# Optimization experiments

Measured on AMD Instinct MI355X. Metric: run time of the kernel, lower is better.

Reference implementation:

```python
import jax, jax.numpy as jnp
import numpy as np

D = 1024      # d_model
H = 16        # n_heads
M = 64        # n_memories
DK = D // H   # head dim
EPS = 1e-5    # LayerNorm eps


def setup_inputs() -> dict:
    key = jax.random.key(0)
    ks = jax.random.split(key, 16)
    B, N = 4, 1024
    s = 0.02
    return {
        "queries": jax.random.normal(ks[0], (B, N, D), jnp.float32),
        "keys": jax.random.normal(ks[1], (B, N, D), jnp.float32),
        "values": jax.random.normal(ks[2], (B, N, D), jnp.float32),
        "attention_mask": jax.random.randint(ks[3], (B, 1, 1, N), 0, 2, dtype=jnp.int32),
        "Wq": jax.random.normal(ks[4], (D, D), jnp.float32) * s,
        "bq": jnp.zeros((D,), jnp.float32),
        "Wk": jax.random.normal(ks[5], (D, D), jnp.float32) * s,
        "bk": jnp.zeros((D,), jnp.float32),
        "Wv": jax.random.normal(ks[6], (D, D), jnp.float32) * s,
        "bv": jnp.zeros((D,), jnp.float32),
        "Wo": jax.random.normal(ks[7], (D, D), jnp.float32) * s,
        "bo": jnp.zeros((D,), jnp.float32),
        "m_k": jax.random.normal(ks[8], (1, M, D), jnp.float32) * 0.01,
        "m_v": jax.random.normal(ks[9], (1, M, D), jnp.float32) * 0.01,
        "gamma": jnp.ones((D,), jnp.float32),
        "beta": jnp.zeros((D,), jnp.float32),
    }


def _layer_norm(x, gamma, beta):
    mu = jnp.mean(x, axis=-1, keepdims=True)
    var = jnp.var(x, axis=-1, keepdims=True)
    return (x - mu) * jax.lax.rsqrt(var + EPS) * gamma + beta


def reference(queries, keys, values, attention_mask,
              Wq, bq, Wk, bk, Wv, bv, Wo, bo, m_k, m_v, gamma, beta):
    B, Nq, _ = queries.shape
    Nk = keys.shape[1]
    scale = 1.0 / np.sqrt(DK)

    # projections (torch Linear: x @ W.T + b)
    q = (queries @ Wq.T + bq).reshape(B, Nq, H, DK).transpose(0, 2, 1, 3)  # b h nq d

    # memory-augmented K/V (memory tokens scaled as in the source)
    k_full = jnp.concatenate(
        [keys @ Wk.T + bk, jnp.broadcast_to(m_k * np.sqrt(DK), (B, M, D))], axis=1)
    v_full = jnp.concatenate(
        [values @ Wv.T + bv, jnp.broadcast_to(m_v * np.sqrt(M), (B, M, D))], axis=1)
    k = k_full.reshape(B, Nk + M, H, DK).transpose(0, 2, 1, 3)  # b h nk+m d
    v = v_full.reshape(B, Nk + M, H, DK).transpose(0, 2, 1, 3)  # b h nk+m d

    scores = jnp.einsum('bhqd,bhkd->bhqk', q, k) * scale  # [B,H,Nq,Nk+M]

    # partial masking: only the first Nk (non-memory) columns are maskable
    mask = jnp.concatenate(
        [attention_mask.astype(bool),
         jnp.zeros((B, 1, 1, M), dtype=bool)], axis=-1)
    scores = jnp.where(mask, -jnp.inf, scores)

    p_attn = jax.nn.softmax(scores, axis=-1)  # dropout p=0.0 -> identity
    out = jnp.einsum('bhqk,bhkd->bhqd', p_attn, v)
    out = out.transpose(0, 2, 1, 3).reshape(B, Nq, D)
    out = out @ Wo.T + bo

    # residual + LayerNorm (outer dropout is identity at p=0.0)
    return _layer_norm(queries + out, gamma, beta)
```

## Files before the change

kernel.cpp:

```cpp
#include <hip/hip_runtime.h>


typedef __bf16 bf16;
typedef __bf16 bf16x8 __attribute__((ext_vector_type(8)));
typedef __bf16 bf16x4 __attribute__((ext_vector_type(4)));
typedef __bf16 bf16x2 __attribute__((ext_vector_type(2)));
typedef float  f32x4  __attribute__((ext_vector_type(4)));
typedef float  f32x16 __attribute__((ext_vector_type(16)));
typedef unsigned uintx4 __attribute__((ext_vector_type(4)));

#define NSEQ 1024
#define NKV  1088
#define DMODEL 1024

struct CvtArgs { const float* s[7]; const float* mk; const float* mv; };

__global__ __launch_bounds__(256) void prep(CvtArgs c, bf16* __restrict__ dst,
                                            bf16* __restrict__ Kb,
                                            bf16* __restrict__ Vt)
{
    int blk = blockIdx.x;
    if (blk < 8192) {
        size_t e = ((size_t)blk * 256 + threadIdx.x) * 8;
        const float* s;
        if (e < ((size_t)3 << 22)) {
            s = c.s[e >> 22] + (e & 0x3FFFFF);
        } else {
            size_t wq = e - ((size_t)3 << 22);
            s = c.s[3 + (wq >> 20)] + (wq & 0xFFFFF);
        }
        f32x4 a = *(const f32x4*)s;
        f32x4 b = *(const f32x4*)(s + 4);
        bf16x8 o;
        for (int i = 0; i < 4; i++) { o[i] = (bf16)a[i]; o[4 + i] = (bf16)b[i]; }
        *(bf16x8*)&dst[e] = o;
    } else {
        int i = (blk - 8192) * 256 + threadIdx.x;
        int b = i >> 16, md = i & 65535;
        int m = md >> 10, dcol = md & 1023;
        Kb[(size_t)b * (NKV * DMODEL) + (size_t)(NSEQ + m) * DMODEL + dcol]
            = (bf16)(c.mk[md] * 8.0f);
        Vt[((size_t)b * 1024 + dcol) * NKV + NSEQ + m] = (bf16)(c.mv[md] * 8.0f);
    }
}

typedef __attribute__((address_space(1))) void gas_void;
typedef __attribute__((address_space(3))) void las_void;

__device__ __forceinline__ void gload16(const bf16* g, bf16* l)
{
    __builtin_amdgcn_global_load_lds((gas_void*)g, (las_void*)l, 16, 0, 0);
}

struct GemmArgsB {
    const bf16* A;
    const bf16* W;
    const float* bias;
    void* C;
    int osK;
    int vt;
    int k0;
};

template<int KLEN>
__device__ __forceinline__ void gemm128_body(const GemmArgsB g, int bx, int by)
{
    __shared__ bf16 As[128][32];
    __shared__ bf16 Bs[128][32];
    const int t = threadIdx.x;
    const int lane = t & 63, w = t >> 6;
    const int qi = lane & 15, qq = lane >> 4;
    const int wrow = (w >> 1) * 64, wcol = (w & 1) * 64;
    const int bm = by * 128, bn = bx * 128;

    const int srow = w * 32 + (lane >> 2);
    const int scol = (lane & 3) * 8;
    const bf16* Ag = g.A + (size_t)(bm + srow) * DMODEL + g.k0 + scol;
    const bf16* Wg = g.W + (size_t)(bn + srow) * DMODEL + g.k0 + scol;
    bf16* Al = &As[w * 32][0];
    bf16* Bl = &Bs[w * 32][0];

    f32x4 acc[4][4] = {};

#define STAGE(kt)                                                             \
    do {                                                                      \
        gload16(Ag + (kt),                 Al);                               \
        gload16(Ag + (kt) + 16 * DMODEL,   Al + 16 * 32);                     \
        gload16(Wg + (kt),                 Bl);                               \
        gload16(Wg + (kt) + 16 * DMODEL,   Bl + 16 * 32);                    \
    } while (0)

    STAGE(0);
    for (int kt = 0; kt < KLEN; kt += 32) {
        __syncthreads();
        bf16x8 a[4], b[4];
        for (int i = 0; i < 4; i++)
            a[i] = *(const bf16x8*)&As[wrow + i * 16 + qi][qq * 8];
        for (int j = 0; j < 4; j++)
            b[j] = *(const bf16x8*)&Bs[wcol + j * 16 + qi][qq * 8];
        __syncthreads();
        if (kt + 32 < KLEN) STAGE(kt + 32);
        for (int i = 0; i < 4; i++)
            for (int j = 0; j < 4; j++)
                acc[i][j] = __builtin_amdgcn_mfma_f32_16x16x32_bf16(
                    a[i], b[j], acc[i][j], 0, 0, 0);
    }
#undef STAGE

    for (int i = 0; i < 4; i++)
        for (int j = 0; j < 4; j++) {
            int row0 = bm + wrow + i * 16 + qq * 4;
            int col  = bn + wcol + j * 16 + qi;
            float bcol = g.bias ? g.bias[col] : 0.0f;
            if (g.vt == 1) {
                bf16x4 v;
                for (int r = 0; r < 4; r++) v[r] = (bf16)(acc[i][j][r] + bcol);
                size_t off = ((size_t)((row0 >> 10) * 16 + (col >> 6)) * 64 + (col & 63))
                           * NKV + (row0 & 1023);
                *(bf16x4*)&((bf16*)g.C)[off] = v;
            } else if (g.vt == 2) {
                float* Cf = (float*)g.C;
                for (int r = 0; r < 4; r++) {
                    int row = row0 + r;
                    Cf[(size_t)row * DMODEL + col] = acc[i][j][r] + bcol;
                }
            } else {
                bf16* Cb = (bf16*)g.C;
                for (int r = 0; r < 4; r++) {
                    int row = row0 + r;
                    size_t off = (size_t)(row >> 10) * g.osK
                               + (size_t)(row & 1023) * DMODEL + col;
                    Cb[off] = (bf16)(acc[i][j][r] + bcol);
                }
            }
        }
}

template<int KLEN>
__global__ __launch_bounds__(256, 3) void gemm128_lds(GemmArgsB g0, GemmArgsB g1,
                                                      GemmArgsB g2)
{
    int bx = blockIdx.x, by = blockIdx.y, bz = blockIdx.z;
    if (gridDim.x == 8 && gridDim.y == 32) {
        int lin = bx + 8 * (by + 32 * bz);
        int k = lin & 7, j = lin >> 3;
        bx = j & 7;
        by = k * 4 + ((j >> 3) & 3);
        bz = j >> 5;
    }
    const GemmArgsB g = (bz == 0) ? g0 : (bz == 1) ? g1 : g2;
    gemm128_body<KLEN>(g, bx, by);
}

struct GemmArgs {
    const void* A;
    const float* W;
    const float* bias;
    bf16* C;
    int osK;
    int vt;
};

template<bool ABF>
__global__ __launch_bounds__(256, 2) void gemm128(GemmArgs g0, GemmArgs g1, GemmArgs g2)
{
    const GemmArgs g = (blockIdx.z == 0) ? g0 : (blockIdx.z == 1) ? g1 : g2;
    __shared__ bf16 As[128][44];
    __shared__ bf16 Bs[128][44];
    const int t = threadIdx.x;
    const int lane = t & 63, w = t >> 6;
    const int qi = lane & 15, qq = lane >> 4;
    const int wrow = (w >> 1) * 64, wcol = (w & 1) * 64;
    const int bm = blockIdx.y * 128, bn = blockIdx.x * 128;
    const int sr = t >> 1, sc = (t & 1) * 16;

    f32x4 acc[4][4] = {};

    f32x4 pa[4];
    bf16x8 pab[2];
    f32x4 pw[4];

    const float* Wp = g.W + (size_t)(bn + sr) * DMODEL + sc;
    const float* Af = (const float*)g.A + (size_t)(bm + sr) * DMODEL + sc;
    const bf16*  Ab = (const bf16*)g.A + (size_t)(bm + sr) * DMODEL + sc;

#define LOAD_TILES(kt)                                                        \
    do {                                                                      \
        if (ABF) {                                                            \
            pab[0] = *(const bf16x8*)(Ab + (kt));                             \
            pab[1] = *(const bf16x8*)(Ab + (kt) + 8);                         \
        } else {                                                              \
            pa[0] = *(const f32x4*)(Af + (kt));                               \
            pa[1] = *(const f32x4*)(Af + (kt) + 4);                           \
            pa[2] = *(const f32x4*)(Af + (kt) + 8);                           \
            pa[3] = *(const f32x4*)(Af + (kt) + 12);                          \
        }                                                                     \
        pw[0] = *(const f32x4*)(Wp + (kt));                                   \
        pw[1] = *(const f32x4*)(Wp + (kt) + 4);                               \
        pw[2] = *(const f32x4*)(Wp + (kt) + 8);                               \
        pw[3] = *(const f32x4*)(Wp + (kt) + 12);                              \
    } while (0)

#define STORE_TILES()                                                         \
    do {                                                                      \
        if (ABF) {                                                            \
            *(bf16x8*)&As[sr][sc]     = pab[0];                               \
            *(bf16x8*)&As[sr][sc + 8] = pab[1];                               \
        } else {                                                              \
            bf16x8 v0, v1;                                                    \
            for (int i = 0; i < 4; i++) {                                     \
                v0[i] = (bf16)pa[0][i]; v0[4 + i] = (bf16)pa[1][i];           \
                v1[i] = (bf16)pa[2][i]; v1[4 + i] = (bf16)pa[3][i];           \
            }                                                                 \
            *(bf16x8*)&As[sr][sc]     = v0;                                   \
            *(bf16x8*)&As[sr][sc + 8] = v1;                                   \
        }                                                                     \
        {                                                                     \
            bf16x8 u0, u1;                                                    \
            for (int i = 0; i < 4; i++) {                                     \
                u0[i] = (bf16)pw[0][i]; u0[4 + i] = (bf16)pw[1][i];           \
                u1[i] = (bf16)pw[2][i]; u1[4 + i] = (bf16)pw[3][i];           \
            }                                                                 \
            *(bf16x8*)&Bs[sr][sc]     = u0;                                   \
            *(bf16x8*)&Bs[sr][sc + 8] = u1;                                   \
        }                                                                     \
    } while (0)

    LOAD_TILES(0);
    STORE_TILES();
    __syncthreads();

    for (int kt = 0; kt < DMODEL; kt += 32) {
        const bool more = (kt + 32) < DMODEL;
        if (more) LOAD_TILES(kt + 32);
        bf16x8 a[4], b[4];
        for (int i = 0; i < 4; i++)
            a[i] = *(const bf16x8*)&As[wrow + i * 16 + qi][qq * 8];
        for (int j = 0; j < 4; j++)
            b[j] = *(const bf16x8*)&Bs[wcol + j * 16 + qi][qq * 8];
        for (int i = 0; i < 4; i++)
            for (int j = 0; j < 4; j++)
                acc[i][j] = __builtin_amdgcn_mfma_f32_16x16x32_bf16(a[i], b[j], acc[i][j], 0, 0, 0);
        if (more) {
            __syncthreads();
            STORE_TILES();
            __syncthreads();
        }
    }
#undef LOAD_TILES
#undef STORE_TILES

    for (int i = 0; i < 4; i++)
        for (int j = 0; j < 4; j++) {
            int row0 = bm + wrow + i * 16 + qq * 4;
            int col  = bn + wcol + j * 16 + qi;
            float bcol = g.bias[col];
            if (g.vt) {
                bf16x4 v;
                for (int r = 0; r < 4; r++) v[r] = (bf16)(acc[i][j][r] + bcol);
                size_t off = ((size_t)((row0 >> 10) * 16 + (col >> 6)) * 64 + (col & 63))
                           * NKV + (row0 & 1023);
                *(bf16x4*)&g.C[off] = v;
            } else {
                for (int r = 0; r < 4; r++) {
                    int row = row0 + r;
                    size_t off = (size_t)(row >> 10) * g.osK
                               + (size_t)(row & 1023) * DMODEL + col;
                    g.C[off] = (bf16)(acc[i][j][r] + bcol);
                }
            }
        }
}

__global__ void fill_mem(const float* __restrict__ mk, const float* __restrict__ mv,
                         bf16* __restrict__ K, bf16* __restrict__ Vt)
{
    int i = blockIdx.x * 256 + threadIdx.x;
    int b = i >> 16, md = i & 65535;
    int m = md >> 10, dcol = md & 1023;
    K[(size_t)b * (NKV * DMODEL) + (size_t)(NSEQ + m) * DMODEL + dcol]
        = (bf16)(mk[md] * 8.0f);
    Vt[((size_t)b * 1024 + dcol) * NKV + NSEQ + m] = (bf16)(mv[md] * 8.0f);
}

__device__ __forceinline__ unsigned pkbf(float a, float b)
{
    bf16x2 t; t[0] = (bf16)a; t[1] = (bf16)b;
    unsigned u; __builtin_memcpy(&u, &t, 4); return u;
}

__global__ __launch_bounds__(256) void attn_flash(const bf16* Q,
        const bf16* __restrict__ K, const bf16* __restrict__ Vt,
        const int* __restrict__ mask, bf16* O)
{
    __shared__ bf16 sKV[2][2][64][72];
    __shared__ __align__(16) float sM[NKV];
    const int t = threadIdx.x, lane = t & 63, w = t >> 6;
    int bh, q0;
    if (gridDim.y == 64) {
        int lin = blockIdx.y * gridDim.x + blockIdx.x;
        bh = ((lin & 7) << 3) | ((lin >> 3) & 7);
        q0 = (lin >> 6) * 128;
    } else {
        bh = blockIdx.y;
        q0 = blockIdx.x * 128;
    }
    const int b = bh >> 4, h = bh & 15;
    const int sr = t >> 2, sc = (t & 3) * 16;
    const int lq = lane & 31, hi = lane >> 5;

    for (int j = t; j < NKV; j += 256)
        sM[j] = (j < NSEQ && mask[b * NSEQ + j] != 0) ? -3.0e38f : 0.0f;

    const size_t qrow = (size_t)(b * NSEQ + q0 + w * 32 + lq) * DMODEL + h * 64;
    bf16x8 qf[4];
#pragma unroll
    for (int c = 0; c < 4; c++) {
        bf16x8 v = *(const bf16x8*)&Q[qrow + c * 16 + hi * 8];
        for (int i = 0; i < 8; i++) v[i] = (bf16)((float)v[i] * 0.125f);
        qf[c] = v;
    }

    const bf16* kbase = K + (size_t)(b * NKV + sr) * DMODEL + h * 64 + sc;
    const bf16* vbase = Vt + ((size_t)bh * 64 + sr) * NKV + sc;

    bf16x8 pk0, pk1, pv0, pv1;
#define LOAD_KV(jt)                                                           \
    do {                                                                      \
        const bf16* kp = kbase + (size_t)(jt) * 64 * DMODEL;                  \
        pk0 = *(const bf16x8*)kp;                                             \
        pk1 = *(const bf16x8*)(kp + 8);                                       \
        const bf16* vp = vbase + (jt) * 64;                                   \
        pv0 = *(const bf16x8*)vp;                                             \
        pv1 = *(const bf16x8*)(vp + 8);                                       \
    } while (0)
#define STORE_KV(bi)                                                          \
    do {                                                                      \
        *(bf16x8*)&sKV[bi][0][sr][sc]     = pk0;                              \
        *(bf16x8*)&sKV[bi][0][sr][sc + 8] = pk1;                              \
        *(bf16x8*)&sKV[bi][1][sr][sc]     = pv0;                              \
        *(bf16x8*)&sKV[bi][1][sr][sc + 8] = pv1;                              \
    } while (0)

    LOAD_KV(0);
    STORE_KV(0);

    float m_i = -1.0e30f, l_i = 0.f;
    f32x16 oacc0 = {}, oacc1 = {};

    for (int jt = 0; jt < 17; jt++) {
        const int j0 = jt * 64;
        const int cb = jt & 1;
        const bool more = jt < 16;
        if (more) LOAD_KV(jt + 1);
        __syncthreads();

        f32x16 accs[2];
#pragma unroll
        for (int kb = 0; kb < 2; kb++) {
#pragma unroll
            for (int g2 = 0; g2 < 4; g2++) {
                f32x4 m4 = *(const f32x4*)&sM[j0 + kb * 32 + 8 * g2 + 4 * hi];
                accs[kb][4 * g2 + 0] = m4[0];
                accs[kb][4 * g2 + 1] = m4[1];
                accs[kb][4 * g2 + 2] = m4[2];
                accs[kb][4 * g2 + 3] = m4[3];
            }
#pragma unroll
            for (int c = 0; c < 4; c++) {
                bf16x8 kf = *(const bf16x8*)&sKV[cb][0][kb * 32 + lq][c * 16 + hi * 8];
                accs[kb] = __builtin_amdgcn_mfma_f32_32x32x16_bf16(
                    kf, qf[c], accs[kb], 0, 0, 0);
            }
        }

        float rm0 = accs[0][0], rm1 = accs[1][0];
#pragma unroll
        for (int r = 1; r < 16; r++) {
            rm0 = fmaxf(rm0, accs[0][r]);
            rm1 = fmaxf(rm1, accs[1][r]);
        }
        float rm = fmaxf(rm0, rm1);
        rm = fmaxf(rm, __shfl_xor(rm, 32, 64));
        if (!__all(rm - m_i <= 8.0f)) {
            float mnew = fmaxf(m_i, rm);
            float alpha = __expf(m_i - mnew);
            m_i = mnew;
            l_i *= alpha;
#pragma unroll
            for (int r = 0; r < 16; r++) { oacc0[r] *= alpha; oacc1[r] *= alpha; }
        }
        float rs0 = 0.f, rs1 = 0.f;
#pragma unroll
        for (int r = 0; r < 16; r++) {
            float p0 = __expf(accs[0][r] - m_i);
            float p1 = __expf(accs[1][r] - m_i);
            accs[0][r] = p0; accs[1][r] = p1;
            rs0 += p0; rs1 += p1;
        }
        float rs = rs0 + rs1;
        rs += __shfl_xor(rs, 32, 64);
        l_i += rs;

        unsigned dwv[16];
#pragma unroll
        for (int kb = 0; kb < 2; kb++)
#pragma unroll
            for (int a = 0; a < 4; a++) {
                dwv[kb * 8 + 2 * a]     = pkbf(accs[kb][4 * a], accs[kb][4 * a + 1]);
                dwv[kb * 8 + 2 * a + 1] = pkbf(accs[kb][4 * a + 2], accs[kb][4 * a + 3]);
            }
        bf16x8 pb[4];
#pragma unroll
        for (int c = 0; c < 4; c++) {
            const int base = (c >> 1) * 8 + (c & 1) * 4;
            unsigned e0 = dwv[base],     e1 = dwv[base + 1];
            unsigned o0 = dwv[base + 2], o1 = dwv[base + 3];
            uintx4 cw;
#if __has_builtin(__builtin_amdgcn_permlane32_swap)
            auto r0 = __builtin_amdgcn_permlane32_swap(e0, o0, false, false);
            auto r1 = __builtin_amdgcn_permlane32_swap(e1, o1, false, false);
            cw[0] = r0[0]; cw[1] = r1[0]; cw[2] = r0[1]; cw[3] = r1[1];
#else
            unsigned s0 = hi ? e0 : o0, s1 = hi ? e1 : o1;
            unsigned k0 = hi ? o0 : e0, k1 = hi ? o1 : e1;
            unsigned x0 = __shfl_xor((int)s0, 32, 64);
            unsigned x1 = __shfl_xor((int)s1, 32, 64);
            cw[0] = hi ? x0 : k0; cw[1] = hi ? x1 : k1;
            cw[2] = hi ? k0 : x0; cw[3] = hi ? k1 : x1;
#endif
            __builtin_memcpy(&pb[c], &cw, 16);
        }

#pragma unroll
        for (int c = 0; c < 4; c++) {
            bf16x8 vf0 = *(const bf16x8*)&sKV[cb][1][lq][c * 16 + hi * 8];
            bf16x8 vf1 = *(const bf16x8*)&sKV[cb][1][32 + lq][c * 16 + hi * 8];
            oacc0 = __builtin_amdgcn_mfma_f32_32x32x16_bf16(vf0, pb[c], oacc0, 0, 0, 0);
            oacc1 = __builtin_amdgcn_mfma_f32_32x32x16_bf16(vf1, pb[c], oacc1, 0, 0, 0);
        }
        if (more) STORE_KV(cb ^ 1);
    }
#undef LOAD_KV
#undef STORE_KV

    float linv = 1.0f / l_i;
    __syncthreads();
    bf16 (*sO)[72] = reinterpret_cast<bf16(*)[72]>(&sKV[0][0][0][0]);
#pragma unroll
    for (int r = 0; r < 16; r++) {
        int dl = (r & 3) + 8 * (r >> 2) + 4 * hi;
        sO[w * 32 + lq][dl]      = (bf16)(oacc0[r] * linv);
        sO[w * 32 + lq][32 + dl] = (bf16)(oacc1[r] * linv);
    }
    __syncthreads();
    {
        int row = t >> 1, ch = (t & 1) * 32;
        bf16* dst = &O[(size_t)(b * NSEQ + q0 + row) * DMODEL + h * 64 + ch];
#pragma unroll
        for (int k = 0; k < 4; k++)
            *(bf16x8*)(dst + k * 8) = *(const bf16x8*)&sO[row][ch + k * 8];
    }
}

__global__ __launch_bounds__(256) void residual_ln2(const float* __restrict__ X,
        const float* __restrict__ Y0, const float* __restrict__ Y1,
        const float* __restrict__ gamma, const float* __restrict__ beta,
        float* __restrict__ out)
{
    __shared__ float red[8];
    int row = blockIdx.x, t = threadIdx.x;
    size_t base = (size_t)row * DMODEL + t * 4;
    f32x4 xv = *(const f32x4*)&X[base];
    f32x4 y0 = *(const f32x4*)&Y0[base];
    f32x4 y1 = *(const f32x4*)&Y1[base];
    float s[4], sum = 0.f, sq = 0.f;
    for (int i = 0; i < 4; i++) {
        s[i] = xv[i] + y0[i] + y1[i];
        sum += s[i]; sq += s[i] * s[i];
    }
    for (int o = 32; o; o >>= 1) { sum += __shfl_xor(sum, o, 64); sq += __shfl_xor(sq, o, 64); }
    if ((t & 63) == 0) { red[t >> 6] = sum; red[4 + (t >> 6)] = sq; }
    __syncthreads();
    sum = red[0] + red[1] + red[2] + red[3];
    sq  = red[4] + red[5] + red[6] + red[7];
    float mean = sum * (1.0f / DMODEL);
    float var  = sq  * (1.0f / DMODEL) - mean * mean;
    float rstd = rsqrtf(var + 1e-5f);
    f32x4 gv = *(const f32x4*)&gamma[t * 4];
    f32x4 bv = *(const f32x4*)&beta[t * 4];
    f32x4 ov;
    for (int i = 0; i < 4; i++)
        ov[i] = (s[i] - mean) * rstd * gv[i] + bv[i];
    *(f32x4*)&out[base] = ov;
}

__global__ __launch_bounds__(256) void residual_ln(const float* __restrict__ X,
        const bf16* __restrict__ Y, const float* __restrict__ gamma,
        const float* __restrict__ beta, float* __restrict__ out)
{
    __shared__ float red[8];
    int row = blockIdx.x, t = threadIdx.x;
    size_t base = (size_t)row * DMODEL + t * 4;
    f32x4  xv = *(const f32x4*)&X[base];
    bf16x4 yv = *(const bf16x4*)&Y[base];
    float s[4], sum = 0.f, sq = 0.f;
    for (int i = 0; i < 4; i++) {
        s[i] = xv[i] + (float)yv[i];
        sum += s[i]; sq += s[i] * s[i];
    }
    for (int o = 32; o; o >>= 1) { sum += __shfl_xor(sum, o, 64); sq += __shfl_xor(sq, o, 64); }
    if ((t & 63) == 0) { red[t >> 6] = sum; red[4 + (t >> 6)] = sq; }
    __syncthreads();
    sum = red[0] + red[1] + red[2] + red[3];
    sq  = red[4] + red[5] + red[6] + red[7];
    float mean = sum * (1.0f / DMODEL);
    float var  = sq  * (1.0f / DMODEL) - mean * mean;
    float rstd = rsqrtf(var + 1e-5f);
    f32x4 gv = *(const f32x4*)&gamma[t * 4];
    f32x4 bv = *(const f32x4*)&beta[t * 4];
    f32x4 ov;
    for (int i = 0; i < 4; i++)
        ov[i] = (s[i] - mean) * rstd * gv[i] + bv[i];
    *(f32x4*)&out[base] = ov;
}

extern "C" void kernel_launch(void* const* d_in, const int* in_sizes, int n_in,
                              void* d_out, int out_size, void* d_ws, size_t ws_size,
                              hipStream_t stream)
{
    const float* queries = (const float*)d_in[0];
    const float* keys    = (const float*)d_in[1];
    const float* values  = (const float*)d_in[2];
    const int*   amask   = (const int*)d_in[3];
    const float* Wq = (const float*)d_in[4];  const float* bq = (const float*)d_in[5];
    const float* Wk = (const float*)d_in[6];  const float* bk = (const float*)d_in[7];
    const float* Wv = (const float*)d_in[8];  const float* bv = (const float*)d_in[9];
    const float* Wo = (const float*)d_in[10]; const float* bo = (const float*)d_in[11];
    const float* mk = (const float*)d_in[12]; const float* mv = (const float*)d_in[13];
    const float* gamma = (const float*)d_in[14]; const float* beta = (const float*)d_in[15];
    float* out = (float*)d_out;

    bf16* Qb = (bf16*)(out + (size_t)2 * 1024 * 1024);
    const size_t SB  = (size_t)NSEQ * DMODEL;
    const size_t KVB = (size_t)NKV * DMODEL;
    dim3 gb(256);

    const size_t need_r10 = (2 * 4 * KVB + 3 * 4 * SB + 4 * SB) * sizeof(bf16);

    if (ws_size >= need_r10) {
        bf16* Kb = (bf16*)d_ws;
        bf16* Vt = Kb + 4 * KVB;
        bf16* Ab = Vt + 4 * KVB;
        bf16* Wb = Ab + 12 * SB;
        float* PR0 = (float*)Ab;
        float* PR1 = (float*)d_ws;

        CvtArgs ca;
        ca.s[0] = queries; ca.s[1] = keys; ca.s[2] = values;
        ca.s[3] = Wq; ca.s[4] = Wk; ca.s[5] = Wv; ca.s[6] = Wo;
        ca.mk = mk; ca.mv = mv;
        prep<<<dim3(8192 + 1024), gb, 0, stream>>>(ca, Ab, Kb, Vt);

        GemmArgsB gq{Ab,          Wb,          bq, Qb, (int)SB,  0, 0};
        GemmArgsB gk{Ab + 4 * SB, Wb + SB,     bk, Kb, (int)KVB, 0, 0};
        GemmArgsB gv{Ab + 8 * SB, Wb + 2 * SB, bv, Vt, 0,        1, 0};
        gemm128_lds<DMODEL><<<dim3(8, 32, 3), gb, 0, stream>>>(gq, gk, gv);

        attn_flash<<<dim3(8, 64), gb, 0, stream>>>(Qb, Kb, Vt, amask, Qb);

        GemmArgsB go0{Qb, Wb + 3 * SB, bo,      PR0, 0, 2, 0};
        GemmArgsB go1{Qb, Wb + 3 * SB, nullptr, PR1, 0, 2, 512};
        gemm128_lds<512><<<dim3(8, 32, 2), gb, 0, stream>>>(go0, go1, go1);

        residual_ln2<<<dim3(4096), gb, 0, stream>>>(queries, PR0, PR1,
                                                    gamma, beta, out);
    } else if (ws_size >= (size_t)2 * 4 * KVB * sizeof(bf16)) {
        bf16* Kb = (bf16*)d_ws;
        bf16* Vt = Kb + 4 * KVB;
        bf16* PR = Kb;

        GemmArgs gq{queries, Wq, bq, Qb, (int)SB,  0};
        GemmArgs gk{keys,    Wk, bk, Kb, (int)KVB, 0};
        GemmArgs gv{values,  Wv, bv, Vt, 0,        1};
        gemm128<false><<<dim3(8, 32, 3), gb, 0, stream>>>(gq, gk, gv);
        fill_mem<<<dim3(1024), gb, 0, stream>>>(mk, mv, Kb, Vt);
        attn_flash<<<dim3(8, 64), gb, 0, stream>>>(Qb, Kb, Vt, amask, Qb);
        GemmArgs go{Qb, Wo, bo, PR, (int)SB, 0};
        gemm128<true><<<dim3(8, 32, 1), gb, 0, stream>>>(go, go, go);
        residual_ln<<<dim3(4096), gb, 0, stream>>>(queries, PR, gamma, beta, out);
    } else {
        bf16* Kb = (bf16*)d_ws;
        bf16* Vt = Kb + KVB;
        bf16* PR = Kb;

        GemmArgs gq{queries, Wq, bq, Qb, (int)SB, 0};
        gemm128<false><<<dim3(8, 32, 1), gb, 0, stream>>>(gq, gq, gq);
        for (int b = 0; b < 4; b++) {
            GemmArgs gk{keys   + b * SB, Wk, bk, Kb, 0, 0};
            GemmArgs gv{values + b * SB, Wv, bv, Vt, 0, 1};
            gemm128<false><<<dim3(8, 8, 2), gb, 0, stream>>>(gk, gv, gv);
            fill_mem<<<dim3(256), gb, 0, stream>>>(mk, mv, Kb, Vt);
            attn_flash<<<dim3(8, 16), gb, 0, stream>>>(Qb + b * SB, Kb, Vt,
                                                       amask + b * NSEQ, Qb + b * SB);
            GemmArgs go{Qb + b * SB, Wo, bo, PR, 0, 0};
            gemm128<true><<<dim3(8, 8, 1), gb, 0, stream>>>(go, go, go);
            residual_ln<<<dim3(1024), gb, 0, stream>>>(queries + b * SB, PR,
                                                       gamma, beta, out + b * SB);
        }
    }
}
```

Before: 227.7 us.

## Fuse fp32-to-bf16 activation conversion into QKV projection GEMM A-tile loads

The prep kernel no longer converts queries/keys/values to bf16 and now converts only the weights and memory tokens. The QKV GEMM reads fp32 activations directly into registers, converts them and stores them to a padded LDS tile, with the next tile's global load overlapped with the MFMA loop. This removes a full write and reread of 12M bf16 activations. The cost is that the async global-to-LDS DMA path is replaced by register staging for A, which adds register pressure and VALU conversion work inside the GEMM.

Measured after the change: 248.7 us. +9.2%, slower.

```diff
diff --git a/kernel.cpp b/kernel.cpp
--- a/kernel.cpp
+++ b/kernel.cpp
@@ -13,29 +13,23 @@
 #define NKV  1088
 #define DMODEL 1024
 
-struct CvtArgs { const float* s[7]; const float* mk; const float* mv; };
-
-__global__ __launch_bounds__(256) void prep(CvtArgs c, bf16* __restrict__ dst,
-                                            bf16* __restrict__ Kb,
-                                            bf16* __restrict__ Vt)
+struct CvtArgs { const float* s[4]; const float* mk; const float* mv; };
+
+__global__ __launch_bounds__(256) void prep_w(CvtArgs c, bf16* __restrict__ dst,
+                                              bf16* __restrict__ Kb,
+                                              bf16* __restrict__ Vt)
 {
     int blk = blockIdx.x;
-    if (blk < 8192) {
+    if (blk < 2048) {
         size_t e = ((size_t)blk * 256 + threadIdx.x) * 8;
-        const float* s;
-        if (e < ((size_t)3 << 22)) {
-            s = c.s[e >> 22] + (e & 0x3FFFFF);
-        } else {
-            size_t wq = e - ((size_t)3 << 22);
-            s = c.s[3 + (wq >> 20)] + (wq & 0xFFFFF);
-        }
+        const float* s = c.s[e >> 20] + (e & 0xFFFFF);
         f32x4 a = *(const f32x4*)s;
         f32x4 b = *(const f32x4*)(s + 4);
         bf16x8 o;
         for (int i = 0; i < 4; i++) { o[i] = (bf16)a[i]; o[4 + i] = (bf16)b[i]; }
         *(bf16x8*)&dst[e] = o;
     } else {
-        int i = (blk - 8192) * 256 + threadIdx.x;
+        int i = (blk - 2048) * 256 + threadIdx.x;
         int b = i >> 16, md = i & 65535;
         int m = md >> 10, dcol = md & 1023;
         Kb[(size_t)b * (NKV * DMODEL) + (size_t)(NSEQ + m) * DMODEL + dcol]
@@ -53,7 +47,7 @@
 }
 
 struct GemmArgsB {
-    const bf16* A;
+    const void* A;
     const bf16* W;
     const float* bias;
     void* C;
@@ -62,10 +56,10 @@
     int k0;
 };
 
-template<int KLEN>
+template<int KLEN, bool AF32>
 __device__ __forceinline__ void gemm128_body(const GemmArgsB g, int bx, int by)
 {
-    __shared__ bf16 As[128][32];
+    __shared__ bf16 As[128][AF32 ? 36 : 32];
     __shared__ bf16 Bs[128][32];
     const int t = threadIdx.x;
     const int lane = t & 63, w = t >> 6;
@@ -75,22 +69,48 @@
 
     const int srow = w * 32 + (lane >> 2);
     const int scol = (lane & 3) * 8;
-    const bf16* Ag = g.A + (size_t)(bm + srow) * DMODEL + g.k0 + scol;
     const bf16* Wg = g.W + (size_t)(bn + srow) * DMODEL + g.k0 + scol;
+    bf16* Bl = &Bs[w * 32][0];
+
+    const int asr = t >> 1, asc = (t & 1) * 16;
+    const float* Af = (const float*)g.A + (size_t)(bm + asr) * DMODEL + g.k0 + asc;
+    const bf16* Ab = (const bf16*)g.A + (size_t)(bm + srow) * DMODEL + g.k0 + scol;
     bf16* Al = &As[w * 32][0];
-    bf16* Bl = &Bs[w * 32][0];
 
     f32x4 acc[4][4] = {};
-
-#define STAGE(kt)                                                             \
-    do {                                                                      \
-        gload16(Ag + (kt),                 Al);                               \
-        gload16(Ag + (kt) + 16 * DMODEL,   Al + 16 * 32);                     \
-        gload16(Wg + (kt),                 Bl);                               \
-        gload16(Wg + (kt) + 16 * DMODEL,   Bl + 16 * 32);                    \
-    } while (0)
-
-    STAGE(0);
+    f32x4 pa[4];
+
+#define STAGE_W(kt)                                                           \
+    do {                                                                      \
+        gload16(Wg + (kt),               Bl);                                 \
+        gload16(Wg + (kt) + 16 * DMODEL, Bl + 16 * 32);                       \
+    } while (0)
+#define STAGE_A_DMA(kt)                                                       \
+    do {                                                                      \
+        gload16(Ab + (kt),               Al);                                 \
+        gload16(Ab + (kt) + 16 * DMODEL, Al + 16 * 32);                       \
+    } while (0)
+#define LOAD_A(kt)                                                            \
+    do {                                                                      \
+        pa[0] = *(const f32x4*)(Af + (kt));                                   \
+        pa[1] = *(const f32x4*)(Af + (kt) + 4);                               \
+        pa[2] = *(const f32x4*)(Af + (kt) + 8);                               \
+        pa[3] = *(const f32x4*)(Af + (kt) + 12);                              \
+    } while (0)
+#define STORE_A()                                                             \
+    do {                                                                      \
+        bf16x8 v0, v1;                                                        \
+        for (int i = 0; i < 4; i++) {                                         \
+            v0[i] = (bf16)pa[0][i]; v0[4 + i] = (bf16)pa[1][i];               \
+            v1[i] = (bf16)pa[2][i]; v1[4 + i] = (bf16)pa[3][i];               \
+        }                                                                     \
+        *(bf16x8*)&As[asr][asc]     = v0;                                     \
+        *(bf16x8*)&As[asr][asc + 8] = v1;                                     \
+    } while (0)
+
+    if (AF32) { LOAD_A(0); STORE_A(); STAGE_W(0); }
+    else      { STAGE_A_DMA(0); STAGE_W(0); }
+
     for (int kt = 0; kt < KLEN; kt += 32) {
         __syncthreads();
         bf16x8 a[4], b[4];
@@ -99,13 +119,22 @@
         for (int j = 0; j < 4; j++)
             b[j] = *(const bf16x8*)&Bs[wcol + j * 16 + qi][qq * 8];
         __syncthreads();
-        if (kt + 32 < KLEN) STAGE(kt + 32);
+        const bool more = kt + 32 < KLEN;
+        if (more) {
+            if (AF32) LOAD_A(kt + 32);
+            else      STAGE_A_DMA(kt + 32);
+            STAGE_W(kt + 32);
+        }
         for (int i = 0; i < 4; i++)
             for (int j = 0; j < 4; j++)
                 acc[i][j] = __builtin_amdgcn_mfma_f32_16x16x32_bf16(
                     a[i], b[j], acc[i][j], 0, 0, 0);
-    }
-#undef STAGE
+        if (more && AF32) STORE_A();
+    }
+#undef STAGE_W
+#undef STAGE_A_DMA
+#undef LOAD_A
+#undef STORE_A
 
     for (int i = 0; i < 4; i++)
         for (int j = 0; j < 4; j++) {
@@ -136,7 +165,7 @@
         }
 }
 
-template<int KLEN>
+template<int KLEN, bool AF32>
 __global__ __launch_bounds__(256, 3) void gemm128_lds(GemmArgsB g0, GemmArgsB g1,
                                                       GemmArgsB g2)
 {
@@ -149,7 +178,7 @@
         bz = j >> 5;
     }
     const GemmArgsB g = (bz == 0) ? g0 : (bz == 1) ? g1 : g2;
-    gemm128_body<KLEN>(g, bx, by);
+    gemm128_body<KLEN, AF32>(g, bx, by);
 }
 
 struct GemmArgs {
@@ -557,21 +586,20 @@
         float* PR1 = (float*)d_ws;
 
         CvtArgs ca;
-        ca.s[0] = queries; ca.s[1] = keys; ca.s[2] = values;
-        ca.s[3] = Wq; ca.s[4] = Wk; ca.s[5] = Wv; ca.s[6] = Wo;
+        ca.s[0] = Wq; ca.s[1] = Wk; ca.s[2] = Wv; ca.s[3] = Wo;
         ca.mk = mk; ca.mv = mv;
-        prep<<<dim3(8192 + 1024), gb, 0, stream>>>(ca, Ab, Kb, Vt);
-
-        GemmArgsB gq{Ab,          Wb,          bq, Qb, (int)SB,  0, 0};
-        GemmArgsB gk{Ab + 4 * SB, Wb + SB,     bk, Kb, (int)KVB, 0, 0};
-        GemmArgsB gv{Ab + 8 * SB, Wb + 2 * SB, bv, Vt, 0,        1, 0};
-        gemm128_lds<DMODEL><<<dim3(8, 32, 3), gb, 0, stream>>>(gq, gk, gv);
+        prep_w<<<dim3(2048 + 1024), gb, 0, stream>>>(ca, Wb, Kb, Vt);
+
+        GemmArgsB gq{queries, Wb,          bq, Qb, (int)SB,  0, 0};
+        GemmArgsB gk{keys,    Wb + SB,     bk, Kb, (int)KVB, 0, 0};
+        GemmArgsB gv{values,  Wb + 2 * SB, bv, Vt, 0,        1, 0};
+        gemm128_lds<DMODEL, true><<<dim3(8, 32, 3), gb, 0, stream>>>(gq, gk, gv);
 
         attn_flash<<<dim3(8, 64), gb, 0, stream>>>(Qb, Kb, Vt, amask, Qb);
 
         GemmArgsB go0{Qb, Wb + 3 * SB, bo,      PR0, 0, 2, 0};
         GemmArgsB go1{Qb, Wb + 3 * SB, nullptr, PR1, 0, 2, 512};
-        gemm128_lds<512><<<dim3(8, 32, 2), gb, 0, stream>>>(go0, go1, go1);
+        gemm128_lds<512, false><<<dim3(8, 32, 2), gb, 0, stream>>>(go0, go1, go1);
 
         residual_ln2<<<dim3(4096), gb, 0, stream>>>(queries, PR0, PR1,
                                                     gamma, beta, out);
```
